# Kernel tuning notes

Measured on AMD Instinct MI355X. Metric: run time of the kernel, lower is better.

## Reference

```python
import jax, jax.numpy as jnp
import numpy as np

B, S, D_MODEL, H = 2, 2048, 1024, 16
DK = D_MODEL // H
THETA = 10000.0


def setup_inputs() -> dict:
    key = jax.random.key(0)
    ks = jax.random.split(key, 5)
    scale = 0.02  # keep logits in a numerically sane range
    return {
        "x": jax.random.normal(ks[0], (B, S, D_MODEL), jnp.float32),
        "Q_weight": jax.random.normal(ks[1], (D_MODEL, D_MODEL), jnp.float32) * scale,
        "K_weight": jax.random.normal(ks[2], (D_MODEL, D_MODEL), jnp.float32) * scale,
        "V_weight": jax.random.normal(ks[3], (D_MODEL, D_MODEL), jnp.float32) * scale,
        "O_weight": jax.random.normal(ks[4], (D_MODEL, D_MODEL), jnp.float32) * scale,
        "token_positions": jnp.arange(S, dtype=jnp.int32),
    }


def _rope(x, token_positions, theta, d_k):
    # x: [..., seq, d_k]; rotate interleaved even/odd pairs
    inv_freq = 1.0 / theta ** (jnp.arange(0, d_k, 2, dtype=jnp.float32) / d_k)
    ang = token_positions.astype(jnp.float32)[:, None] * inv_freq  # [S, d_k/2]
    cos, sin = jnp.cos(ang), jnp.sin(ang)
    x0, x1 = x[..., 0::2], x[..., 1::2]
    y0 = x0 * cos - x1 * sin
    y1 = x0 * sin + x1 * cos
    return jnp.stack([y0, y1], axis=-1).reshape(x.shape)


def _mhsa(x, Qw, Kw, Vw, Ow, token_positions):
    b, s, d = x.shape
    qw = Qw.reshape(H, DK, d)
    kw = Kw.reshape(H, DK, d)
    vw = Vw.reshape(H, DK, d)
    q = jnp.einsum('hki,bsi->bhsk', qw, x)
    k = jnp.einsum('hki,bsi->bhsk', kw, x)
    v = jnp.einsum('hvi,bsi->bhsv', vw, x)
    q = _rope(q, token_positions, THETA, DK)
    k = _rope(k, token_positions, THETA, DK)
    scores = jnp.einsum('bhnd,bhmd->bhnm', q, k) / jnp.sqrt(jnp.float32(DK))
    causal = jnp.tril(jnp.ones((s, s), dtype=bool))
    scores = jnp.where(causal, scores, -jnp.inf)
    attn = jax.nn.softmax(scores, axis=-1)
    o = jnp.einsum('bhnm,bhmv->bhnv', attn, v)  # [B,H,S,DV]
    o = jnp.transpose(o, (0, 2, 1, 3)).reshape(b, s, H * DK)
    return jnp.einsum('dv,bsv->bsd', Ow, o)


def reference(x, Q_weight, K_weight, V_weight, O_weight, token_positions):
    return _mhsa(x, Q_weight, K_weight, V_weight, O_weight, token_positions)
```

## Files before the change

### kernel.cpp

```cpp
#include <hip/hip_runtime.h>

#define NB 2
#define NS 2048
#define NDM 1024
#define NH 16
#define NDK 64

typedef unsigned int u32;
typedef u32 u32x4 __attribute__((ext_vector_type(4)));
typedef float f32x4 __attribute__((ext_vector_type(4)));
typedef float f32x2 __attribute__((ext_vector_type(2)));
typedef __bf16 bf16x8 __attribute__((ext_vector_type(8)));
typedef __bf16 bf16x4 __attribute__((ext_vector_type(4)));
typedef __bf16 bf16x2 __attribute__((ext_vector_type(2)));

#define QSCALE 0.18033688011112042f
#define EXP2F(x) __builtin_amdgcn_exp2f(x)

__device__ __forceinline__ void gload_lds16(const __bf16* g, __bf16* l) {
    __builtin_amdgcn_global_load_lds(
        (const __attribute__((address_space(1))) unsigned int*)(g),
        (__attribute__((address_space(3))) unsigned int*)(l), 16, 0, 0);
}

__global__ __launch_bounds__(256) void cvt_all(const float* __restrict__ x,
                                               const float* __restrict__ qw,
                                               const float* __restrict__ kw,
                                               const float* __restrict__ vw,
                                               const float* __restrict__ ow,
                                               const int* __restrict__ tp,
                                               __bf16* __restrict__ xb,
                                               __bf16* __restrict__ wqkv,
                                               __bf16* __restrict__ owb,
                                               float* __restrict__ tbl) {
    const int i = blockIdx.x * 256 + threadIdx.x;
    if (i >= 2097152) {
        const int it = i - 2097152;
        if (it < NS * 32) {
            const int s = it >> 5, jj = it & 31;
            const float pos = (float)tp[s];
            const float inv = exp2f(-0.41524101186092f * (float)jj);
            const float ang = pos * inv;
            float sn, cs;
            sincosf(ang, &sn, &cs);
            f32x2 o; o[0] = cs; o[1] = sn;
            *(f32x2*)&tbl[(size_t)it * 2] = o;
        }
        return;
    }
    const float* src;
    __bf16* dst;
    if (i < 1048576) {
        src = x + (size_t)i * 4;
        dst = xb + (size_t)i * 4;
    } else {
        const int j = i - 1048576;
        const int seg = j >> 18;
        const int off = j & 0x3FFFF;
        src = ((seg == 0) ? qw : (seg == 1) ? kw : (seg == 2) ? vw : ow) + (size_t)off * 4;
        dst = ((seg == 3) ? owb : wqkv + (size_t)seg * 1048576) + (size_t)off * 4;
    }
    f32x4 v = *(const f32x4*)src;
    bf16x4 o;
    o[0] = (__bf16)v[0]; o[1] = (__bf16)v[1]; o[2] = (__bf16)v[2]; o[3] = (__bf16)v[3];
    *(bf16x4*)dst = o;
}

__global__ __launch_bounds__(256) void gemm_qkv128(const __bf16* __restrict__ A,
                                                   const __bf16* __restrict__ Bt,
                                                   __bf16* __restrict__ C,
                                                   __bf16* __restrict__ Vt) {
    __shared__ __bf16 As[2][128 * 64];
    __shared__ __bf16 Bs[2][128 * 64];
    const int K = 1024, lda = 1024, ldb = 1024, ldc = 3072;
    const int tid = threadIdx.x;
    const int lane = tid & 63, w = tid >> 6;
    const int wr = w >> 1, wc = w & 1;
    const int l15 = lane & 15, lg = lane >> 4;
    const int m0 = blockIdx.y * 128, n0 = blockIdx.x * 128;
    const int crow = lane >> 3;
    const int csw = ((lane & 7) ^ crow) * 8;

    f32x4 acc[4][4];
    const f32x4 z = {0.f, 0.f, 0.f, 0.f};
#pragma unroll
    for (int i = 0; i < 4; ++i)
#pragma unroll
        for (int jx = 0; jx < 4; ++jx) acc[i][jx] = z;

    auto stage = [&](int buf, int k0) {
#pragma unroll
        for (int ch = 0; ch < 4; ++ch) {
            const int cid = w * 4 + ch;
            const int ra = cid * 8 + crow;
            gload_lds16(&A[(size_t)(m0 + ra) * lda + k0 + csw], &As[buf][cid * 512]);
            gload_lds16(&Bt[(size_t)(n0 + ra) * ldb + k0 + csw], &Bs[buf][cid * 512]);
        }
    };

    stage(0, 0);
    int cur = 0;
    for (int k0 = 0; k0 < K; k0 += 64) {
        if (k0 + 64 < K) {
            stage(cur ^ 1, k0 + 64);
            asm volatile("s_waitcnt vmcnt(8)" ::: "memory");
        } else {
            asm volatile("s_waitcnt vmcnt(0)" ::: "memory");
        }
        __builtin_amdgcn_s_barrier();
        __builtin_amdgcn_sched_barrier(0);
#pragma unroll
        for (int kc = 0; kc < 2; ++kc) {
            bf16x8 af[4], bfv[4];
#pragma unroll
            for (int i = 0; i < 4; ++i) {
                const int ra = wr * 64 + i * 16 + l15;
                const int rb = wc * 64 + i * 16 + l15;
                af[i]  = *(const bf16x8*)&As[cur][ra * 64 + ((kc * 32 + lg * 8) ^ ((ra & 7) << 3))];
                bfv[i] = *(const bf16x8*)&Bs[cur][rb * 64 + ((kc * 32 + lg * 8) ^ ((rb & 7) << 3))];
            }
#pragma unroll
            for (int sm = 0; sm < 4; ++sm)
#pragma unroll
                for (int sn = 0; sn < 4; ++sn)
                    acc[sm][sn] = __builtin_amdgcn_mfma_f32_16x16x32_bf16(af[sm], bfv[sn], acc[sm][sn], 0, 0, 0);
        }
        asm volatile("s_waitcnt lgkmcnt(0)" ::: "memory");
        __builtin_amdgcn_s_barrier();
        __builtin_amdgcn_sched_barrier(0);
        cur ^= 1;
    }
    if (n0 < 2048) {
#pragma unroll
        for (int sm = 0; sm < 4; ++sm)
#pragma unroll
            for (int sn = 0; sn < 4; ++sn)
#pragma unroll
                for (int j = 0; j < 4; ++j) {
                    const int row = m0 + wr * 64 + sm * 16 + lg * 4 + j;
                    const int col = n0 + wc * 64 + sn * 16 + l15;
                    C[(size_t)row * ldc + col] = (__bf16)acc[sm][sn][j];
                }
    } else {
#pragma unroll
        for (int sm = 0; sm < 4; ++sm)
#pragma unroll
            for (int sn = 0; sn < 4; ++sn) {
                const int col = (n0 - 2048) + wc * 64 + sn * 16 + l15;
                const int h = col >> 6, d = col & 63;
                const int row = m0 + wr * 64 + sm * 16 + lg * 4;
                const int b = row >> 11, s = row & (NS - 1);
                bf16x4 ov;
#pragma unroll
                for (int j = 0; j < 4; ++j) ov[j] = (__bf16)acc[sm][sn][j];
                *(bf16x4*)&Vt[((size_t)(b * NH + h) * 64 + d) * NS + s] = ov;
            }
    }
}

template <typename TOUT>
__global__ __launch_bounds__(256) void gemm_bt128(const __bf16* __restrict__ A,
                                                  const __bf16* __restrict__ Bt,
                                                  TOUT* __restrict__ C,
                                                  int K, int lda, int ldb, int ldc) {
    __shared__ __bf16 As[2][128 * 64];
    __shared__ __bf16 Bs[2][128 * 64];
    const int tid = threadIdx.x;
    const int lane = tid & 63, w = tid >> 6;
    const int wr = w >> 1, wc = w & 1;
    const int l15 = lane & 15, lg = lane >> 4;
    const int m0 = blockIdx.y * 128, n0 = blockIdx.x * 128;
    const int crow = lane >> 3;
    const int csw = ((lane & 7) ^ crow) * 8;

    f32x4 acc[4][4];
    const f32x4 z = {0.f, 0.f, 0.f, 0.f};
#pragma unroll
    for (int i = 0; i < 4; ++i)
#pragma unroll
        for (int jx = 0; jx < 4; ++jx) acc[i][jx] = z;

    auto stage = [&](int buf, int k0) {
#pragma unroll
        for (int ch = 0; ch < 4; ++ch) {
            const int cid = w * 4 + ch;
            const int ra = cid * 8 + crow;
            gload_lds16(&A[(size_t)(m0 + ra) * lda + k0 + csw], &As[buf][cid * 512]);
            gload_lds16(&Bt[(size_t)(n0 + ra) * ldb + k0 + csw], &Bs[buf][cid * 512]);
        }
    };

    stage(0, 0);
    int cur = 0;
    for (int k0 = 0; k0 < K; k0 += 64) {
        if (k0 + 64 < K) {
            stage(cur ^ 1, k0 + 64);
            asm volatile("s_waitcnt vmcnt(8)" ::: "memory");
        } else {
            asm volatile("s_waitcnt vmcnt(0)" ::: "memory");
        }
        __builtin_amdgcn_s_barrier();
        __builtin_amdgcn_sched_barrier(0);
#pragma unroll
        for (int kc = 0; kc < 2; ++kc) {
            bf16x8 af[4], bfv[4];
#pragma unroll
            for (int i = 0; i < 4; ++i) {
                const int ra = wr * 64 + i * 16 + l15;
                const int rb = wc * 64 + i * 16 + l15;
                af[i]  = *(const bf16x8*)&As[cur][ra * 64 + ((kc * 32 + lg * 8) ^ ((ra & 7) << 3))];
                bfv[i] = *(const bf16x8*)&Bs[cur][rb * 64 + ((kc * 32 + lg * 8) ^ ((rb & 7) << 3))];
            }
#pragma unroll
            for (int sm = 0; sm < 4; ++sm)
#pragma unroll
                for (int sn = 0; sn < 4; ++sn)
                    acc[sm][sn] = __builtin_amdgcn_mfma_f32_16x16x32_bf16(af[sm], bfv[sn], acc[sm][sn], 0, 0, 0);
        }
        asm volatile("s_waitcnt lgkmcnt(0)" ::: "memory");
        __builtin_amdgcn_s_barrier();
        __builtin_amdgcn_sched_barrier(0);
        cur ^= 1;
    }
#pragma unroll
    for (int sm = 0; sm < 4; ++sm)
#pragma unroll
        for (int sn = 0; sn < 4; ++sn)
#pragma unroll
            for (int j = 0; j < 4; ++j) {
                const int row = m0 + wr * 64 + sm * 16 + lg * 4 + j;
                const int col = n0 + wc * 64 + sn * 16 + l15;
                C[(size_t)row * ldc + col] = (TOUT)acc[sm][sn][j];
            }
}

__global__ __launch_bounds__(512) void rope_kernel(const __bf16* __restrict__ qkv,
                                                   const float* __restrict__ tbl,
                                                   __bf16* __restrict__ Qr,
                                                   __bf16* __restrict__ Kr) {
    const int row = blockIdx.x;
    const int s = row & (NS - 1);
    const int b = row >> 11;
    const int t = threadIdx.x;
    const int h = t >> 5, jj = t & 31;
    f32x2 cssn = *(const f32x2*)&tbl[((size_t)s * 32 + jj) * 2];
    const float cs = cssn[0], sn = cssn[1];
    const __bf16* qp = qkv + (size_t)row * 3072 + h * 64 + 2 * jj;
    bf16x2 qv = *(const bf16x2*)qp;
    bf16x2 kv = *(const bf16x2*)(qp + 1024);
    const float q0 = (float)qv[0], q1 = (float)qv[1];
    const float k0 = (float)kv[0], k1 = (float)kv[1];
    const size_t o = ((size_t)(b * NH + h) * NS + s) * 64 + 2 * jj;
    bf16x2 qo, ko;
    qo[0] = (__bf16)((q0 * cs - q1 * sn) * QSCALE);
    qo[1] = (__bf16)((q0 * sn + q1 * cs) * QSCALE);
    ko[0] = (__bf16)(k0 * cs - k1 * sn); ko[1] = (__bf16)(k0 * sn + k1 * cs);
    *(bf16x2*)&Qr[o] = qo;
    *(bf16x2*)&Kr[o] = ko;
}

__device__ __forceinline__ int kperm(int rt) {
    const int ct = rt >> 4, rr = rt & 15;
    return ((rr >> 2) << 3) + ((ct >> 1) << 5) + ((ct & 1) << 2) + (rr & 3);
}

__global__ __launch_bounds__(256) void attn5(const __bf16* __restrict__ Qr,
                                             const __bf16* __restrict__ Kr,
                                             const __bf16* __restrict__ Vt,
                                             __bf16* __restrict__ O) {
    const int lid = blockIdx.x;
    const int xcd = lid & 7;
    const int g = lid >> 3;
    const int bh = xcd * 4 + (g & 3);
    const int pr = g >> 2;
    const int p = (pr < 8) ? (pr * 2) : (31 - 2 * pr);
    const int b = bh >> 4, h = bh & 15;
    const int tid = threadIdx.x;
    const int w = tid >> 6, lane = tid & 63;
    const int l15 = lane & 15, lg = lane >> 4;
    const __bf16* Qb = Qr + (size_t)bh * NS * 64;
    const __bf16* Kb = Kr + (size_t)bh * NS * 64;
    const __bf16* Vb = Vt + (size_t)bh * 64 * NS;

    __shared__ __bf16 Ks[2][64 * 64];
    __shared__ __bf16 Vs[2][64 * 64];

    const int rbv[2] = {p * 64 + w * 16, (31 - p) * 64 + w * 16};

    bf16x8 qf[2][2];
#pragma unroll
    for (int rs = 0; rs < 2; ++rs)
#pragma unroll
        for (int kc = 0; kc < 2; ++kc)
            qf[rs][kc] = *(const bf16x8*)(Qb + (size_t)(rbv[rs] + l15) * 64 + kc * 32 + lg * 8);

    f32x4 oacc[2][4];
    const f32x4 z = {0.f, 0.f, 0.f, 0.f};
#pragma unroll
    for (int rs = 0; rs < 2; ++rs)
#pragma unroll
        for (int ct = 0; ct < 4; ++ct) oacc[rs][ct] = z;
    float lsum[2] = {0.f, 0.f};

    const int crow = lane >> 3;
    const int cswz = ((lane & 7) ^ crow) * 8;

#pragma unroll
    for (int pp = 0; pp < 2; ++pp) {
        const int ch = w + pp * 4;
        const int rt = ch * 8 + crow;
        gload_lds16(Kb + (size_t)kperm(rt) * 64 + cswz, &Ks[0][ch * 512]);
        gload_lds16(Vb + (size_t)rt * NS + 0 + cswz, &Vs[0][ch * 512]);
    }
    __syncthreads();

    const int nt = 32 - p;
    for (int t = 0; t < nt; ++t) {
        const int cur = t & 1;
        const int kv0 = t << 6;
        if (t + 1 < nt) {
            const int kv1 = kv0 + 64;
#pragma unroll
            for (int pp = 0; pp < 2; ++pp) {
                const int ch = w + pp * 4;
                const int rt = ch * 8 + crow;
                gload_lds16(Kb + (size_t)(kv1 + kperm(rt)) * 64 + cswz, &Ks[cur ^ 1][ch * 512]);
                gload_lds16(Vb + (size_t)rt * NS + kv1 + cswz, &Vs[cur ^ 1][ch * 512]);
            }
        }
        bool act[2];
        act[0] = (kv0 <= rbv[0] + 15);
        act[1] = true;
        f32x4 sc[2][4];
#pragma unroll
        for (int rs = 0; rs < 2; ++rs)
            if (act[rs])
#pragma unroll
                for (int ct = 0; ct < 4; ++ct) sc[rs][ct] = z;
#pragma unroll
        for (int kc = 0; kc < 2; ++kc) {
            bf16x8 kf[4];
#pragma unroll
            for (int ct = 0; ct < 4; ++ct) {
                const int rt = ct * 16 + l15;
                kf[ct] = *(const bf16x8*)&Ks[cur][rt * 64 + ((kc * 32 + lg * 8) ^ ((rt & 7) << 3))];
            }
#pragma unroll
            for (int rs = 0; rs < 2; ++rs)
                if (act[rs])
#pragma unroll
                    for (int ct = 0; ct < 4; ++ct)
                        sc[rs][ct] = __builtin_amdgcn_mfma_f32_16x16x32_bf16(kf[ct], qf[rs][kc], sc[rs][ct], 0, 0, 0);
        }
        bf16x8 pb[2][2];
#pragma unroll
        for (int rs = 0; rs < 2; ++rs) {
            if (!act[rs]) continue;
            const int rbase = rbv[rs];
            const int qrow = rbase + l15;
            const bool needmask = (kv0 + 63 > rbase);
            if (needmask) {
#pragma unroll
                for (int ct = 0; ct < 4; ++ct)
#pragma unroll
                    for (int j = 0; j < 4; ++j) {
                        const int kvg = kv0 + ((ct >> 1) << 5) + lg * 8 + ((ct & 1) << 2) + j;
                        if (kvg > qrow) sc[rs][ct][j] = -1e30f;
                    }
            }
            float ps = 0.f;
#pragma unroll
            for (int ct = 0; ct < 4; ++ct)
#pragma unroll
                for (int j = 0; j < 4; ++j) {
                    const float e = EXP2F(sc[rs][ct][j]);
                    sc[rs][ct][j] = e;
                    ps += e;
                }
            lsum[rs] += ps;
#pragma unroll
            for (int kc = 0; kc < 2; ++kc) {
                bf16x8 pk;
                pk[0] = (__bf16)sc[rs][2 * kc][0];     pk[1] = (__bf16)sc[rs][2 * kc][1];
                pk[2] = (__bf16)sc[rs][2 * kc][2];     pk[3] = (__bf16)sc[rs][2 * kc][3];
                pk[4] = (__bf16)sc[rs][2 * kc + 1][0]; pk[5] = (__bf16)sc[rs][2 * kc + 1][1];
                pk[6] = (__bf16)sc[rs][2 * kc + 1][2]; pk[7] = (__bf16)sc[rs][2 * kc + 1][3];
                pb[rs][kc] = pk;
            }
        }
#pragma unroll
        for (int kc = 0; kc < 2; ++kc) {
            bf16x8 vf[4];
#pragma unroll
            for (int ct = 0; ct < 4; ++ct) {
                const int rt = ct * 16 + l15;
                vf[ct] = *(const bf16x8*)&Vs[cur][rt * 64 + ((kc * 32 + lg * 8) ^ ((rt & 7) << 3))];
            }
#pragma unroll
            for (int rs = 0; rs < 2; ++rs) {
                if (!act[rs]) continue;
#pragma unroll
                for (int ct = 0; ct < 4; ++ct)
                    oacc[rs][ct] = __builtin_amdgcn_mfma_f32_16x16x32_bf16(vf[ct], pb[rs][kc], oacc[rs][ct], 0, 0, 0);
            }
        }
        __syncthreads();
    }
#pragma unroll
    for (int rs = 0; rs < 2; ++rs) {
        float tot = lsum[rs];
        tot += __shfl_xor(tot, 16, 64);
        tot += __shfl_xor(tot, 32, 64);
        const float rl = 1.0f / tot;
        const size_t rowoff = (size_t)(b * NS + rbv[rs] + l15) * NDM + h * 64 + lg * 4;
#pragma unroll
        for (int ct = 0; ct < 4; ++ct) {
            bf16x4 ov;
#pragma unroll
            for (int j = 0; j < 4; ++j) ov[j] = (__bf16)(oacc[rs][ct][j] * rl);
            *(bf16x4*)&O[rowoff + ct * 16] = ov;
        }
    }
}

extern "C" void kernel_launch(void* const* d_in, const int* in_sizes, int n_in,
                              void* d_out, int out_size, void* d_ws, size_t ws_size,
                              hipStream_t stream) {
    const float* x  = (const float*)d_in[0];
    const float* Qw = (const float*)d_in[1];
    const float* Kw = (const float*)d_in[2];
    const float* Vw = (const float*)d_in[3];
    const float* Ow = (const float*)d_in[4];
    const int*   tp = (const int*)d_in[5];
    float* out = (float*)d_out;

    char* ws = (char*)d_ws;
    size_t off = 0;
    auto alloc = [&](size_t bytes) -> void* {
        void* p = ws + off;
        off += (bytes + 255) & ~(size_t)255;
        return p;
    };
    __bf16* xb   = (__bf16*)alloc((size_t)4096 * 1024 * 2);
    __bf16* wqkv = (__bf16*)alloc((size_t)3072 * 1024 * 2);
    __bf16* owb  = (__bf16*)alloc((size_t)1024 * 1024 * 2);
    __bf16* qkv  = (__bf16*)alloc((size_t)4096 * 3072 * 2);
    __bf16* qr   = (__bf16*)alloc((size_t)32 * 2048 * 64 * 2);
    __bf16* kr   = (__bf16*)alloc((size_t)32 * 2048 * 64 * 2);
    __bf16* vt   = (__bf16*)alloc((size_t)32 * 64 * 2048 * 2);
    __bf16* ob   = (__bf16*)alloc((size_t)4096 * 1024 * 2);
    float*  tbl  = (float*)alloc((size_t)NS * 32 * 2 * 4);

    cvt_all<<<8448, 256, 0, stream>>>(x, Qw, Kw, Vw, Ow, tp, xb, wqkv, owb, tbl);

    gemm_qkv128<<<dim3(3072 / 128, 4096 / 128), 256, 0, stream>>>(xb, wqkv, qkv, vt);
    rope_kernel<<<4096, 512, 0, stream>>>(qkv, tbl, qr, kr);
    attn5<<<dim3(512), 256, 0, stream>>>(qr, kr, vt, ob);
    gemm_bt128<float><<<dim3(1024 / 128, 4096 / 128), 256, 0, stream>>>(
        ob, owb, out, 1024, 1024, 1024, 1024);
}
```

Before: 117.6 us.

## Fuse RoPE into QKV GEMM epilogue via permuted weight rows

Reorders the Q and K weight rows during conversion so that each head's even features land in the first 32 output columns and its odd features in the last 32. A single thread then holds both members of every RoPE pair in its accumulators. The GEMM epilogue applies the rotation (and the Q scale) and writes Qr/Kr directly in head-major layout. This removes the separate rope kernel and the round trip through the intermediate qkv buffer. The cost is extra table loads and scattered bf16x2 stores in the GEMM epilogue.

```diff
diff --git a/kernel.cpp b/kernel.cpp
--- a/kernel.cpp
+++ b/kernel.cpp
@@ -58,7 +58,15 @@
         const int seg = j >> 18;
         const int off = j & 0x3FFFF;
         src = ((seg == 0) ? qw : (seg == 1) ? kw : (seg == 2) ? vw : ow) + (size_t)off * 4;
-        dst = ((seg == 3) ? owb : wqkv + (size_t)seg * 1048576) + (size_t)off * 4;
+        if (seg <= 1) {
+            const int row = off >> 8;
+            const int c4 = off & 255;
+            const int h = row >> 6, fr = row & 63;
+            const int pr = (fr >> 1) | ((fr & 1) << 5);
+            dst = wqkv + (((size_t)(seg << 10) + h * 64 + pr) << 10) + (size_t)c4 * 4;
+        } else {
+            dst = ((seg == 3) ? owb : wqkv + (size_t)seg * 1048576) + (size_t)off * 4;
+        }
     }
     f32x4 v = *(const f32x4*)src;
     bf16x4 o;
@@ -68,11 +76,13 @@
 
 __global__ __launch_bounds__(256) void gemm_qkv128(const __bf16* __restrict__ A,
                                                    const __bf16* __restrict__ Bt,
-                                                   __bf16* __restrict__ C,
+                                                   const float* __restrict__ tbl,
+                                                   __bf16* __restrict__ Qr,
+                                                   __bf16* __restrict__ Kr,
                                                    __bf16* __restrict__ Vt) {
     __shared__ __bf16 As[2][128 * 64];
     __shared__ __bf16 Bs[2][128 * 64];
-    const int K = 1024, lda = 1024, ldb = 1024, ldc = 3072;
+    const int K = 1024, lda = 1024, ldb = 1024;
     const int tid = threadIdx.x;
     const int lane = tid & 63, w = tid >> 6;
     const int wr = w >> 1, wc = w & 1;
@@ -131,16 +141,28 @@
         cur ^= 1;
     }
     if (n0 < 2048) {
+        __bf16* dst = (n0 < 1024) ? Qr : Kr;
+        const float scale = (n0 < 1024) ? QSCALE : 1.0f;
+        const int h = ((n0 & 1023) + wc * 64) >> 6;
 #pragma unroll
         for (int sm = 0; sm < 4; ++sm)
 #pragma unroll
-            for (int sn = 0; sn < 4; ++sn)
-#pragma unroll
-                for (int j = 0; j < 4; ++j) {
-                    const int row = m0 + wr * 64 + sm * 16 + lg * 4 + j;
-                    const int col = n0 + wc * 64 + sn * 16 + l15;
-                    C[(size_t)row * ldc + col] = (__bf16)acc[sm][sn][j];
+            for (int j = 0; j < 4; ++j) {
+                const int row = m0 + wr * 64 + sm * 16 + lg * 4 + j;
+                const int b = row >> 11, s = row & (NS - 1);
+                const size_t base = ((size_t)(b * NH + h) * NS + s) * 64;
+#pragma unroll
+                for (int pp = 0; pp < 2; ++pp) {
+                    const int jj = pp * 16 + l15;
+                    f32x2 cssn = *(const f32x2*)&tbl[((size_t)s * 32 + jj) * 2];
+                    const float e  = acc[sm][pp][j];
+                    const float od = acc[sm][pp + 2][j];
+                    bf16x2 ov;
+                    ov[0] = (__bf16)((e * cssn[0] - od * cssn[1]) * scale);
+                    ov[1] = (__bf16)((e * cssn[1] + od * cssn[0]) * scale);
+                    *(bf16x2*)&dst[base + 2 * jj] = ov;
                 }
+            }
     } else {
 #pragma unroll
         for (int sm = 0; sm < 4; ++sm)
@@ -232,31 +254,6 @@
                 const int col = n0 + wc * 64 + sn * 16 + l15;
                 C[(size_t)row * ldc + col] = (TOUT)acc[sm][sn][j];
             }
-}
-
-__global__ __launch_bounds__(512) void rope_kernel(const __bf16* __restrict__ qkv,
-                                                   const float* __restrict__ tbl,
-                                                   __bf16* __restrict__ Qr,
-                                                   __bf16* __restrict__ Kr) {
-    const int row = blockIdx.x;
-    const int s = row & (NS - 1);
-    const int b = row >> 11;
-    const int t = threadIdx.x;
-    const int h = t >> 5, jj = t & 31;
-    f32x2 cssn = *(const f32x2*)&tbl[((size_t)s * 32 + jj) * 2];
-    const float cs = cssn[0], sn = cssn[1];
-    const __bf16* qp = qkv + (size_t)row * 3072 + h * 64 + 2 * jj;
-    bf16x2 qv = *(const bf16x2*)qp;
-    bf16x2 kv = *(const bf16x2*)(qp + 1024);
-    const float q0 = (float)qv[0], q1 = (float)qv[1];
-    const float k0 = (float)kv[0], k1 = (float)kv[1];
-    const size_t o = ((size_t)(b * NH + h) * NS + s) * 64 + 2 * jj;
-    bf16x2 qo, ko;
-    qo[0] = (__bf16)((q0 * cs - q1 * sn) * QSCALE);
-    qo[1] = (__bf16)((q0 * sn + q1 * cs) * QSCALE);
-    ko[0] = (__bf16)(k0 * cs - k1 * sn); ko[1] = (__bf16)(k0 * sn + k1 * cs);
-    *(bf16x2*)&Qr[o] = qo;
-    *(bf16x2*)&Kr[o] = ko;
 }
 
 __device__ __forceinline__ int kperm(int rt) {
@@ -444,7 +441,6 @@
     __bf16* xb   = (__bf16*)alloc((size_t)4096 * 1024 * 2);
     __bf16* wqkv = (__bf16*)alloc((size_t)3072 * 1024 * 2);
     __bf16* owb  = (__bf16*)alloc((size_t)1024 * 1024 * 2);
-    __bf16* qkv  = (__bf16*)alloc((size_t)4096 * 3072 * 2);
     __bf16* qr   = (__bf16*)alloc((size_t)32 * 2048 * 64 * 2);
     __bf16* kr   = (__bf16*)alloc((size_t)32 * 2048 * 64 * 2);
     __bf16* vt   = (__bf16*)alloc((size_t)32 * 64 * 2048 * 2);
@@ -453,8 +449,7 @@
 
     cvt_all<<<8448, 256, 0, stream>>>(x, Qw, Kw, Vw, Ow, tp, xb, wqkv, owb, tbl);
 
-    gemm_qkv128<<<dim3(3072 / 128, 4096 / 128), 256, 0, stream>>>(xb, wqkv, qkv, vt);
-    rope_kernel<<<4096, 512, 0, stream>>>(qkv, tbl, qr, kr);
+    gemm_qkv128<<<dim3(3072 / 128, 4096 / 128), 256, 0, stream>>>(xb, wqkv, tbl, qr, kr, vt);
     attn5<<<dim3(512), 256, 0, stream>>>(qr, kr, vt, ob);
     gemm_bt128<float><<<dim3(1024 / 128, 4096 / 128), 256, 0, stream>>>(
         ob, owb, out, 1024, 1024, 1024, 1024);
```

Measured after the change: 112.6 us. 4.2% less time.
